# Kernel optimization log

Measured on AMD Instinct MI355X. Metric: run time of the kernel, lower is better.

Reference implementation:

```python
import jax, jax.numpy as jnp
import numpy as np

NEG_BIG = -1e9

def setup_inputs() -> dict:
    key = jax.random.key(0)
    kq, kk, kv, kwq, kwk, kwv, km = jax.random.split(key, 7)
    B, S, d = 16, 1024, 512
    Q = jax.random.normal(kq, (B, S, d), dtype=jnp.float32)
    K = jax.random.normal(kk, (B, S, d), dtype=jnp.float32)
    V = jax.random.normal(kv, (B, S, d), dtype=jnp.float32)
    # nn.Linear weights [d, d]; torch applies x @ W.T
    WQ = jax.random.normal(kwq, (d, d), dtype=jnp.float32) / np.sqrt(d)
    WK = jax.random.normal(kwk, (d, d), dtype=jnp.float32) / np.sqrt(d)
    WV = jax.random.normal(kwv, (d, d), dtype=jnp.float32) / np.sqrt(d)
    mask = jax.random.randint(km, (B, S), 0, 2, dtype=jnp.int32)
    return {"Q": Q, "K": K, "V": V, "WQ": WQ, "WK": WK, "WV": WV, "mask": mask}


def reference(Q, K, V, WQ, WK, WV, mask):
    d = Q.shape[-1]
    q = jnp.einsum('bsd,ed->bse', Q, WQ)
    k = jnp.einsum('bsd,ed->bse', K, WK)
    v = jnp.einsum('bsd,ed->bse', V, WV)
    scores = jnp.einsum('bqd,bkd->bqk', q, k) / jnp.sqrt(jnp.float32(d))
    attn = jax.nn.softmax(scores, axis=-1)
    # Faithful to original: mask applied AFTER softmax with -1e9 fill
    m = mask[:, None, :]  # [B,1,S] broadcast over query dim
    attn = jnp.where(m == 0, jnp.float32(NEG_BIG), attn)
    out = jnp.einsum('bqk,bkd->bqd', attn, v)
    return (out, attn)
```

## Files before the change

kernel.cpp:

```cpp
#include <hip/hip_runtime.h>
#include <hip/hip_bf16.h>

typedef float f32x4 __attribute__((ext_vector_type(4)));
typedef __bf16 bf16x8 __attribute__((ext_vector_type(8)));
typedef unsigned short u16x8 __attribute__((ext_vector_type(8)));
typedef unsigned short u16x4 __attribute__((ext_vector_type(4)));
typedef int i32x4 __attribute__((ext_vector_type(4)));

#define NEG_BIG_F (-1000000000.0f)
#define SCALE_F 0.044194173824159216f

__device__ __forceinline__ unsigned short f2bf(float f) {
  unsigned int u = __float_as_uint(f);
  u += 0x7FFFu + ((u >> 16) & 1u);
  return (unsigned short)(u >> 16);
}

__device__ __forceinline__ float bf2f(unsigned short h) {
  return __uint_as_float((unsigned int)h << 16);
}

__device__ __forceinline__ u16x8 cvt8(f32x4 a, f32x4 b) {
  u16x8 r;
  r[0] = f2bf(a[0]); r[1] = f2bf(a[1]); r[2] = f2bf(a[2]); r[3] = f2bf(a[3]);
  r[4] = f2bf(b[0]); r[5] = f2bf(b[1]); r[6] = f2bf(b[2]); r[7] = f2bf(b[3]);
  return r;
}

__device__ __forceinline__ bf16x8 u2b(u16x8 u) {
  union { u16x8 u; bf16x8 b; } c; c.u = u; return c.b;
}

__device__ __forceinline__ void gload16(const void* g, char* l) {
  __builtin_amdgcn_global_load_lds(
      (const __attribute__((address_space(1))) unsigned int*)g,
      (__attribute__((address_space(3))) unsigned int*)l, 16, 0, 0);
}

__global__ __launch_bounds__(256) void cvtWX(
    const float* __restrict__ w0, const float* __restrict__ w1,
    const float* __restrict__ w2, const float* __restrict__ Q,
    const float* __restrict__ Kx,
    unsigned short* __restrict__ wb, unsigned short* __restrict__ xb)
{
  const int z = blockIdx.z;
  if (z == 0) {
    if (blockIdx.x >= 384) return;
    const int i = (blockIdx.x * 256 + threadIdx.x) * 8;
    const float* src = i < 262144 ? w0 : (i < 524288 ? w1 : w2);
    const int j = i & 262143;
    f32x4 a = *(const f32x4*)(src + j);
    f32x4 b = *(const f32x4*)(src + j + 4);
    *(u16x8*)&wb[i] = cvt8(a, b);
  } else {
    const float* src = z == 1 ? Q : Kx;
    unsigned short* dst = xb + (size_t)(z - 1) * 8388608;
    const int i = (blockIdx.x * 256 + threadIdx.x) * 8;
    f32x4 a = *(const f32x4*)(src + i);
    f32x4 b = *(const f32x4*)(src + i + 4);
    *(u16x8*)&dst[i] = cvt8(a, b);
  }
}

__global__ __launch_bounds__(512, 2) void proj_all(
    const unsigned short* __restrict__ xb, const float* __restrict__ V,
    const unsigned short* __restrict__ wb,
    unsigned short* __restrict__ qb, unsigned short* __restrict__ kb,
    unsigned short* __restrict__ vt)
{
  __shared__ __align__(16) char pool[81920];

  const int bid = blockIdx.x;
  const int tid = threadIdx.x;
  const int lane = tid & 63, wave = tid >> 6;
  const int fr = lane & 15, fq = lane >> 4;

  if (bid < 256) {
    unsigned short (*As)[256][32] = (unsigned short (*)[256][32])pool;
    unsigned short (*Bs)[256][32] = (unsigned short (*)[256][32])(pool + 32768);

    const int z = bid >> 7, rem = bid & 127;
    const int m0 = (rem & 63) * 256, n0 = (rem >> 6) * 256;
    const unsigned short* Abase = xb + (size_t)z * 8388608 + (size_t)m0 * 512;
    const unsigned short* Bbase = wb + (size_t)z * 262144 + (size_t)n0 * 512;
    const int wr = (wave >> 2) * 128, wc = (wave & 3) * 64;

    f32x4 acc[8][4] = {};

    const unsigned short* gA[2]; char* lA[2];
    const unsigned short* gB[2]; char* lB[2];
    #pragma unroll
    for (int i = 0; i < 2; i++) {
      const int c = tid + 512 * i, row = c >> 2, slot = c & 3;
      const int sw = (slot ^ ((row >> 1) & 3)) * 8;
      gA[i] = Abase + (size_t)row * 512 + sw;
      gB[i] = Bbase + (size_t)row * 512 + sw;
      lA[i] = pool + c * 16;
      lB[i] = pool + 32768 + c * 16;
    }

    #pragma unroll
    for (int i = 0; i < 2; i++) { gload16(gA[i], lA[i]); gload16(gB[i], lB[i]); }

    int cur = 0;
    for (int kt = 0; kt < 512; kt += 32) {
      const int nb = cur ^ 1;
      if (kt < 480) {
        #pragma unroll
        for (int i = 0; i < 2; i++) {
          gload16(gA[i] + kt + 32, lA[i] + nb * 16384);
          gload16(gB[i] + kt + 32, lB[i] + nb * 16384);
        }
        asm volatile("s_waitcnt vmcnt(4) lgkmcnt(0)" ::: "memory");
      } else {
        asm volatile("s_waitcnt vmcnt(0) lgkmcnt(0)" ::: "memory");
      }
      __builtin_amdgcn_sched_barrier(0);
      __builtin_amdgcn_s_barrier();

      bf16x8 bv[4];
      #pragma unroll
      for (int nf = 0; nf < 4; nf++) {
        const int br = wc + nf * 16 + fr;
        bv[nf] = *(const bf16x8*)&Bs[cur][br][(fq ^ ((br >> 1) & 3)) * 8];
      }
      #pragma unroll
      for (int mf = 0; mf < 8; mf++) {
        const int ar = wr + mf * 16 + fr;
        bf16x8 av = *(const bf16x8*)&As[cur][ar][(fq ^ ((ar >> 1) & 3)) * 8];
        #pragma unroll
        for (int nf = 0; nf < 4; nf++)
          acc[mf][nf] = __builtin_amdgcn_mfma_f32_16x16x32_bf16(av, bv[nf], acc[mf][nf], 0, 0, 0);
      }
      __builtin_amdgcn_s_barrier();
      cur = nb;
    }

    unsigned short* Y = z ? kb : qb;
    #pragma unroll
    for (int mf = 0; mf < 8; mf++)
      #pragma unroll
      for (int nf = 0; nf < 4; nf++)
        #pragma unroll
        for (int rr = 0; rr < 4; rr++) {
          const int m = m0 + wr + mf * 16 + fq * 4 + rr;
          const int n = n0 + wc + nf * 16 + fr;
          Y[(size_t)m * 512 + n] = f2bf(acc[mf][nf][rr]);
        }
  } else {
    unsigned short (*As)[128][32] = (unsigned short (*)[128][32])pool;
    float          (*Bf)[256][32] = (float (*)[256][32])(pool + 16384);

    const int bid2 = bid - 256;
    const int m0 = (bid2 & 3) * 128, n0 = ((bid2 >> 2) & 3) * 256, b = bid2 >> 4;
    const int wr = (wave >> 2) * 64, wc = (wave & 3) * 64;
    const unsigned short* wv = wb + 524288;

    f32x4 acc[4][4] = {};

    const int arw = tid >> 2, asl = tid & 3;
    const unsigned short* gA = wv + (size_t)(m0 + arw) * 512 + (asl ^ ((arw >> 1) & 3)) * 8;
    char* lA = pool + tid * 16;
    const float* gB[4]; char* lB[4];
    #pragma unroll
    for (int i = 0; i < 4; i++) {
      const int c = tid + 512 * i, row = c >> 3, slot = c & 7;
      gB[i] = V + ((size_t)b * 1024 + n0 + row) * 512 + (slot ^ (row & 7)) * 4;
      lB[i] = pool + 16384 + c * 16;
    }

    gload16(gA, lA);
    #pragma unroll
    for (int i = 0; i < 4; i++) gload16(gB[i], lB[i]);

    int cur = 0;
    for (int kt = 0; kt < 512; kt += 32) {
      const int nb = cur ^ 1;
      if (kt < 480) {
        gload16(gA + kt + 32, lA + nb * 8192);
        #pragma unroll
        for (int i = 0; i < 4; i++) gload16(gB[i] + kt + 32, lB[i] + nb * 32768);
        asm volatile("s_waitcnt vmcnt(5) lgkmcnt(0)" ::: "memory");
      } else {
        asm volatile("s_waitcnt vmcnt(0) lgkmcnt(0)" ::: "memory");
      }
      __builtin_amdgcn_sched_barrier(0);
      __builtin_amdgcn_s_barrier();

      bf16x8 av[4], bv[4];
      #pragma unroll
      for (int mf = 0; mf < 4; mf++) {
        const int ar = wr + mf * 16 + fr;
        av[mf] = *(const bf16x8*)&As[cur][ar][(fq ^ ((ar >> 1) & 3)) * 8];
      }
      #pragma unroll
      for (int nf = 0; nf < 4; nf++) {
        const int br = wc + nf * 16 + fr;
        f32x4 lo = *(const f32x4*)&Bf[cur][br][((fq * 2)     ^ (br & 7)) * 4];
        f32x4 hi = *(const f32x4*)&Bf[cur][br][((fq * 2 + 1) ^ (br & 7)) * 4];
        bv[nf] = u2b(cvt8(lo, hi));
      }
      #pragma unroll
      for (int mf = 0; mf < 4; mf++)
        #pragma unroll
        for (int nf = 0; nf < 4; nf++)
          acc[mf][nf] = __builtin_amdgcn_mfma_f32_16x16x32_bf16(av[mf], bv[nf], acc[mf][nf], 0, 0, 0);
      __builtin_amdgcn_s_barrier();
      cur = nb;
    }

    #pragma unroll
    for (int mf = 0; mf < 4; mf++)
      #pragma unroll
      for (int nf = 0; nf < 4; nf++)
        #pragma unroll
        for (int rr = 0; rr < 4; rr++) {
          const int e = m0 + wr + mf * 16 + fq * 4 + rr;
          const int s = n0 + wc + nf * 16 + fr;
          vt[((size_t)b * 512 + e) * 1024 + s] = f2bf(acc[mf][nf][rr]);
        }
  }
}

__global__ __launch_bounds__(512, 2) void score_mv(
    const unsigned short* __restrict__ qb, const unsigned short* __restrict__ kb,
    const unsigned short* __restrict__ vt, const int* __restrict__ mask,
    unsigned short* __restrict__ P, float* __restrict__ partial,
    float* __restrict__ mvsum)
{
  __shared__ __align__(16) unsigned short As[2][256][32];
  __shared__ __align__(16) unsigned short Bs[2][256][32];

  const int bid = blockIdx.x;
  const int tid = threadIdx.x;

  if (bid >= 256) {
    const int row = (bid - 256) * 8 + (tid >> 6);
    const int b = row >> 9;
    const int lane = tid & 63;
    const unsigned short* vr = vt + (size_t)row * 1024 + lane * 16;
    const int* mr = mask + b * 1024 + lane * 16;
    u16x8 v0 = *(const u16x8*)(vr);
    u16x8 v1 = *(const u16x8*)(vr + 8);
    float s = 0.f;
    #pragma unroll
    for (int j = 0; j < 8; j++) {
      if (!mr[j])     s += bf2f(v0[j]);
      if (!mr[8 + j]) s += bf2f(v1[j]);
    }
    #pragma unroll
    for (int o = 32; o > 0; o >>= 1) s += __shfl_xor(s, o);
    if (lane == 0) mvsum[row] = s;
    return;
  }

  const int xcd = bid & 7, idx = bid >> 3;
  const int bz = xcd * 2 + (idx >> 4);
  const int tile = idx & 15;
  const int m0 = (tile & 3) * 256, n0 = ((tile >> 2) & 3) * 256;
  const int lane = tid & 63, wave = tid >> 6;
  const int wr = (wave >> 2) * 128, wc = (wave & 3) * 64;
  const int fr = lane & 15, fq = lane >> 4;

  f32x4 acc[8][4] = {};

  const unsigned short* gA[2]; char* lA[2];
  const unsigned short* gB[2]; char* lB[2];
  #pragma unroll
  for (int i = 0; i < 2; i++) {
    const int c = tid + 512 * i, row = c >> 2, slot = c & 3;
    const int sw = (slot ^ ((row >> 1) & 3)) * 8;
    gA[i] = qb + ((size_t)bz * 1024 + m0 + row) * 512 + sw;
    gB[i] = kb + ((size_t)bz * 1024 + n0 + row) * 512 + sw;
    lA[i] = (char*)&As[0][0][0] + c * 16;
    lB[i] = (char*)&Bs[0][0][0] + c * 16;
  }

  #pragma unroll
  for (int i = 0; i < 2; i++) { gload16(gA[i], lA[i]); gload16(gB[i], lB[i]); }

  int cur = 0;
  for (int kt = 0; kt < 512; kt += 32) {
    const int nb = cur ^ 1;
    if (kt < 480) {
      #pragma unroll
      for (int i = 0; i < 2; i++) {
        gload16(gA[i] + kt + 32, lA[i] + nb * 16384);
        gload16(gB[i] + kt + 32, lB[i] + nb * 16384);
      }
      asm volatile("s_waitcnt vmcnt(4) lgkmcnt(0)" ::: "memory");
    } else {
      asm volatile("s_waitcnt vmcnt(0) lgkmcnt(0)" ::: "memory");
    }
    __builtin_amdgcn_sched_barrier(0);
    __builtin_amdgcn_s_barrier();

    bf16x8 bv[4];
    #pragma unroll
    for (int nf = 0; nf < 4; nf++) {
      const int br = wc + nf * 16 + fr;
      bv[nf] = *(const bf16x8*)&Bs[cur][br][(fq ^ ((br >> 1) & 3)) * 8];
    }
    #pragma unroll
    for (int mf = 0; mf < 8; mf++) {
      const int ar = wr + mf * 16 + fr;
      bf16x8 av = *(const bf16x8*)&As[cur][ar][(fq ^ ((ar >> 1) & 3)) * 8];
      #pragma unroll
      for (int nf = 0; nf < 4; nf++)
        acc[mf][nf] = __builtin_amdgcn_mfma_f32_16x16x32_bf16(av, bv[nf], acc[mf][nf], 0, 0, 0);
    }
    __builtin_amdgcn_s_barrier();
    cur = nb;
  }

  int mcol[4];
  #pragma unroll
  for (int nf = 0; nf < 4; nf++)
    mcol[nf] = mask[bz * 1024 + n0 + wc + nf * 16 + fr];

  unsigned short* Pb = P + ((size_t)bz << 20);
  const int slot = ((tile >> 2) & 3) * 4 + (wave & 3);
  #pragma unroll
  for (int mf = 0; mf < 8; mf++) {
    #pragma unroll
    for (int rr = 0; rr < 4; rr++) {
      const int m = m0 + wr + mf * 16 + fq * 4 + rr;
      float e = 0.f;
      #pragma unroll
      for (int nf = 0; nf < 4; nf++) {
        const float ev = __expf(acc[mf][nf][rr] * SCALE_F);
        e += ev;
        Pb[(size_t)m * 1024 + n0 + wc + nf * 16 + fr] =
            mcol[nf] ? f2bf(ev) : (unsigned short)0;
      }
      e += __shfl_xor(e, 1); e += __shfl_xor(e, 2);
      e += __shfl_xor(e, 4); e += __shfl_xor(e, 8);
      if (fr == 0)
        partial[(size_t)slot * 16384 + bz * 1024 + m] = e;
    }
  }
}

__global__ __launch_bounds__(512) void pv_attn(
    const unsigned short* __restrict__ P, const unsigned short* __restrict__ vt,
    const float* __restrict__ partial, const float* __restrict__ mvsum,
    const int* __restrict__ mask,
    float* __restrict__ out, float* __restrict__ attn)
{
  __shared__ __align__(16) unsigned short As[2][64][32];
  __shared__ __align__(16) unsigned short Bs[2][512][32];
  __shared__ float inv_l[64];

  const int tid = threadIdx.x;
  const int lin = blockIdx.x;
  const int xcd = lin & 7, idx = lin >> 3;
  const int bz = xcd * 2 + (idx >> 4);
  const int m0 = (idx & 15) * 64;
  const int lane = tid & 63, wave = tid >> 6;
  const int n0 = wave * 64;
  const int fr = lane & 15, fq = lane >> 4;

  f32x4 acc[4][4] = {};

  if (tid < 64) {
    float s = 0.f;
    #pragma unroll
    for (int p = 0; p < 16; p++) s += partial[(size_t)p * 16384 + bz * 1024 + m0 + tid];
    inv_l[tid] = 1.0f / s;
  }

  const unsigned short* gA = nullptr; char* lA = nullptr;
  if (tid < 256) {
    const int row = tid >> 2, slot = tid & 3;
    gA = P + ((size_t)bz << 20) + (size_t)(m0 + row) * 1024 + (slot ^ ((row >> 1) & 3)) * 8;
    lA = (char*)&As[0][0][0] + tid * 16;
  }
  const unsigned short* gB[4]; char* lB[4];
  #pragma unroll
  for (int i = 0; i < 4; i++) {
    const int c = tid + 512 * i, row = c >> 2, slot = c & 3;
    gB[i] = vt + ((size_t)bz * 512 + row) * 1024 + (slot ^ ((row >> 1) & 3)) * 8;
    lB[i] = (char*)&Bs[0][0][0] + c * 16;
  }

  const int arow = tid >> 3, acol = (tid & 7) * 4;
  const int aslot8 = ((acol >> 3) ^ ((arow >> 1) & 3)) * 8 + (acol & 7);
  float* arp = attn + ((size_t)bz * 1024 + m0 + arow) * 1024 + acol;
  const int* mrp = mask + bz * 1024 + acol;

  if (tid < 256) gload16(gA, lA);
  #pragma unroll
  for (int i = 0; i < 4; i++) gload16(gB[i], lB[i]);
  __syncthreads();

  int cur = 0;
  for (int t = 0; t < 32; t++) {
    const int nb = cur ^ 1;
    const int kt = t * 32;
    if (t < 31) {
      if (tid < 256) gload16(gA + kt + 32, lA + nb * 4096);
      #pragma unroll
      for (int i = 0; i < 4; i++) gload16(gB[i] + kt + 32, lB[i] + nb * 32768);
      if (wave < 4) asm volatile("s_waitcnt vmcnt(5) lgkmcnt(0)" ::: "memory");
      else          asm volatile("s_waitcnt vmcnt(4) lgkmcnt(0)" ::: "memory");
    } else {
      asm volatile("s_waitcnt vmcnt(0) lgkmcnt(0)" ::: "memory");
    }
    __builtin_amdgcn_sched_barrier(0);
    __builtin_amdgcn_s_barrier();

    bf16x8 af[4], bv[4];
    #pragma unroll
    for (int mf = 0; mf < 4; mf++) {
      const int ar = mf * 16 + fr;
      af[mf] = *(const bf16x8*)&As[cur][ar][(fq ^ ((ar >> 1) & 3)) * 8];
    }
    #pragma unroll
    for (int nf = 0; nf < 4; nf++) {
      const int br = n0 + nf * 16 + fr;
      bv[nf] = *(const bf16x8*)&Bs[cur][br][(fq ^ ((br >> 1) & 3)) * 8];
    }
    #pragma unroll
    for (int mf = 0; mf < 4; mf++)
      #pragma unroll
      for (int nf = 0; nf < 4; nf++)
        acc[mf][nf] = __builtin_amdgcn_mfma_f32_16x16x32_bf16(af[mf], bv[nf], acc[mf][nf], 0, 0, 0);

    {
      const u16x4 pv4 = *(const u16x4*)&As[cur][arow][aslot8];
      const i32x4 mv = *(const i32x4*)(mrp + kt);
      const float iv = inv_l[arow];
      f32x4 o;
      o[0] = mv[0] ? bf2f(pv4[0]) * iv : NEG_BIG_F;
      o[1] = mv[1] ? bf2f(pv4[1]) * iv : NEG_BIG_F;
      o[2] = mv[2] ? bf2f(pv4[2]) * iv : NEG_BIG_F;
      o[3] = mv[3] ? bf2f(pv4[3]) * iv : NEG_BIG_F;
      *(f32x4*)(arp + kt) = o;
    }
    __builtin_amdgcn_s_barrier();
    cur = nb;
  }

  float mvv[4];
  #pragma unroll
  for (int nf = 0; nf < 4; nf++)
    mvv[nf] = mvsum[bz * 512 + n0 + nf * 16 + fr];
  #pragma unroll
  for (int mf = 0; mf < 4; mf++)
    #pragma unroll
    for (int rr = 0; rr < 4; rr++) {
      const int m = m0 + mf * 16 + fq * 4 + rr;
      const float iv = inv_l[mf * 16 + fq * 4 + rr];
      #pragma unroll
      for (int nf = 0; nf < 4; nf++)
        out[((size_t)bz * 1024 + m) * 512 + n0 + nf * 16 + fr] =
            iv * acc[mf][nf][rr] + NEG_BIG_F * mvv[nf];
    }
}

extern "C" void kernel_launch(void* const* d_in, const int* in_sizes, int n_in,
                              void* d_out, int out_size, void* d_ws, size_t ws_size,
                              hipStream_t stream)
{
  const float* Q  = (const float*)d_in[0];
  const float* Kx = (const float*)d_in[1];
  const float* V  = (const float*)d_in[2];
  const float* WQ = (const float*)d_in[3];
  const float* WK = (const float*)d_in[4];
  const float* WV = (const float*)d_in[5];
  const int* mask = (const int*)d_in[6];

  const int B = 16, S = 1024, D = 512;
  float* out_f  = (float*)d_out;
  float* attn_f = out_f + (size_t)B * S * D;
  unsigned short* Pbuf = (unsigned short*)d_out;
  unsigned short* xb = (unsigned short*)attn_f;

  unsigned short* qb = (unsigned short*)d_ws;
  unsigned short* kb = qb + (size_t)B * S * D;
  unsigned short* vt = kb + (size_t)B * S * D;
  unsigned short* wb = vt + (size_t)B * S * D;
  float* partial = (float*)(wb + 786432);
  float* mvsum = partial + 262144;

  cvtWX<<<dim3(4096, 1, 3), 256, 0, stream>>>(WQ, WK, WV, Q, Kx, wb, xb);
  proj_all<<<dim3(512), 512, 0, stream>>>(xb, V, wb, qb, kb, vt);
  score_mv<<<dim3(1280), 512, 0, stream>>>(qb, kb, vt, mask, Pbuf, partial, mvsum);
  pv_attn<<<dim3(256), 512, 0, stream>>>(Pbuf, vt, partial, mvsum, mask, out_f, attn_f);
}
```

Measured before the change: 137.2 us.

## Fuse Q/K fp32-to-bf16 conversion into projection GEMM loads

```diff
diff --git a/kernel.cpp b/kernel.cpp
--- a/kernel.cpp
+++ b/kernel.cpp
@@ -37,34 +37,21 @@
       (__attribute__((address_space(3))) unsigned int*)l, 16, 0, 0);
 }
 
-__global__ __launch_bounds__(256) void cvtWX(
+__global__ __launch_bounds__(256) void cvtW(
     const float* __restrict__ w0, const float* __restrict__ w1,
-    const float* __restrict__ w2, const float* __restrict__ Q,
-    const float* __restrict__ Kx,
-    unsigned short* __restrict__ wb, unsigned short* __restrict__ xb)
+    const float* __restrict__ w2, unsigned short* __restrict__ wb)
 {
-  const int z = blockIdx.z;
-  if (z == 0) {
-    if (blockIdx.x >= 384) return;
-    const int i = (blockIdx.x * 256 + threadIdx.x) * 8;
-    const float* src = i < 262144 ? w0 : (i < 524288 ? w1 : w2);
-    const int j = i & 262143;
-    f32x4 a = *(const f32x4*)(src + j);
-    f32x4 b = *(const f32x4*)(src + j + 4);
-    *(u16x8*)&wb[i] = cvt8(a, b);
-  } else {
-    const float* src = z == 1 ? Q : Kx;
-    unsigned short* dst = xb + (size_t)(z - 1) * 8388608;
-    const int i = (blockIdx.x * 256 + threadIdx.x) * 8;
-    f32x4 a = *(const f32x4*)(src + i);
-    f32x4 b = *(const f32x4*)(src + i + 4);
-    *(u16x8*)&dst[i] = cvt8(a, b);
-  }
+  const int i = (blockIdx.x * 256 + threadIdx.x) * 8;
+  const float* src = i < 262144 ? w0 : (i < 524288 ? w1 : w2);
+  const int j = i & 262143;
+  f32x4 a = *(const f32x4*)(src + j);
+  f32x4 b = *(const f32x4*)(src + j + 4);
+  *(u16x8*)&wb[i] = cvt8(a, b);
 }
 
 __global__ __launch_bounds__(512, 2) void proj_all(
-    const unsigned short* __restrict__ xb, const float* __restrict__ V,
-    const unsigned short* __restrict__ wb,
+    const float* __restrict__ Q, const float* __restrict__ Kx,
+    const float* __restrict__ V, const unsigned short* __restrict__ wb,
     unsigned short* __restrict__ qb, unsigned short* __restrict__ kb,
     unsigned short* __restrict__ vt)
 {
@@ -75,27 +62,31 @@
   const int lane = tid & 63, wave = tid >> 6;
   const int fr = lane & 15, fq = lane >> 4;
 
-  if (bid < 256) {
-    unsigned short (*As)[256][32] = (unsigned short (*)[256][32])pool;
+  if (bid < 512) {
+    float          (*Af)[128][32] = (float (*)[128][32])pool;
     unsigned short (*Bs)[256][32] = (unsigned short (*)[256][32])(pool + 32768);
 
-    const int z = bid >> 7, rem = bid & 127;
-    const int m0 = (rem & 63) * 256, n0 = (rem >> 6) * 256;
-    const unsigned short* Abase = xb + (size_t)z * 8388608 + (size_t)m0 * 512;
-    const unsigned short* Bbase = wb + (size_t)z * 262144 + (size_t)n0 * 512;
-    const int wr = (wave >> 2) * 128, wc = (wave & 3) * 64;
-
-    f32x4 acc[8][4] = {};
-
-    const unsigned short* gA[2]; char* lA[2];
+    const int z = bid >> 8, rem = bid & 255;
+    const float* X = z ? Kx : Q;
+    const unsigned short* W = wb + (size_t)z * 262144;
+    unsigned short* Y = z ? kb : qb;
+    const int m0 = (rem >> 1) * 128, n0 = (rem & 1) * 256;
+    const int wr = (wave >> 2) * 64, wc = (wave & 3) * 64;
+
+    f32x4 acc[4][4] = {};
+
+    const float* gA[2]; char* lA[2];
+    #pragma unroll
+    for (int i = 0; i < 2; i++) {
+      const int c = tid + 512 * i, row = c >> 3, slot = c & 7;
+      gA[i] = X + (size_t)(m0 + row) * 512 + (slot ^ (row & 7)) * 4;
+      lA[i] = pool + c * 16;
+    }
     const unsigned short* gB[2]; char* lB[2];
     #pragma unroll
     for (int i = 0; i < 2; i++) {
       const int c = tid + 512 * i, row = c >> 2, slot = c & 3;
-      const int sw = (slot ^ ((row >> 1) & 3)) * 8;
-      gA[i] = Abase + (size_t)row * 512 + sw;
-      gB[i] = Bbase + (size_t)row * 512 + sw;
-      lA[i] = pool + c * 16;
+      gB[i] = W + (size_t)(n0 + row) * 512 + (slot ^ ((row >> 1) & 3)) * 8;
       lB[i] = pool + 32768 + c * 16;
     }
 
@@ -118,27 +109,30 @@
       __builtin_amdgcn_sched_barrier(0);
       __builtin_amdgcn_s_barrier();
 
-      bf16x8 bv[4];
+      bf16x8 av[4], bv[4];
       #pragma unroll
       for (int nf = 0; nf < 4; nf++) {
         const int br = wc + nf * 16 + fr;
         bv[nf] = *(const bf16x8*)&Bs[cur][br][(fq ^ ((br >> 1) & 3)) * 8];
       }
       #pragma unroll
-      for (int mf = 0; mf < 8; mf++) {
+      for (int mf = 0; mf < 4; mf++) {
         const int ar = wr + mf * 16 + fr;
-        bf16x8 av = *(const bf16x8*)&As[cur][ar][(fq ^ ((ar >> 1) & 3)) * 8];
+        f32x4 lo = *(const f32x4*)&Af[cur][ar][((fq * 2)     ^ (ar & 7)) * 4];
+        f32x4 hi = *(const f32x4*)&Af[cur][ar][((fq * 2 + 1) ^ (ar & 7)) * 4];
+        av[mf] = u2b(cvt8(lo, hi));
+      }
+      #pragma unroll
+      for (int mf = 0; mf < 4; mf++)
         #pragma unroll
         for (int nf = 0; nf < 4; nf++)
-          acc[mf][nf] = __builtin_amdgcn_mfma_f32_16x16x32_bf16(av, bv[nf], acc[mf][nf], 0, 0, 0);
-      }
+          acc[mf][nf] = __builtin_amdgcn_mfma_f32_16x16x32_bf16(av[mf], bv[nf], acc[mf][nf], 0, 0, 0);
       __builtin_amdgcn_s_barrier();
       cur = nb;
     }
 
-    unsigned short* Y = z ? kb : qb;
-    #pragma unroll
-    for (int mf = 0; mf < 8; mf++)
+    #pragma unroll
+    for (int mf = 0; mf < 4; mf++)
       #pragma unroll
       for (int nf = 0; nf < 4; nf++)
         #pragma unroll
@@ -151,7 +145,7 @@
     unsigned short (*As)[128][32] = (unsigned short (*)[128][32])pool;
     float          (*Bf)[256][32] = (float (*)[256][32])(pool + 16384);
 
-    const int bid2 = bid - 256;
+    const int bid2 = bid - 512;
     const int m0 = (bid2 & 3) * 128, n0 = ((bid2 >> 2) & 3) * 256, b = bid2 >> 4;
     const int wr = (wave >> 2) * 64, wc = (wave & 3) * 64;
     const unsigned short* wv = wb + 524288;
@@ -474,7 +468,6 @@
   float* out_f  = (float*)d_out;
   float* attn_f = out_f + (size_t)B * S * D;
   unsigned short* Pbuf = (unsigned short*)d_out;
-  unsigned short* xb = (unsigned short*)attn_f;
 
   unsigned short* qb = (unsigned short*)d_ws;
   unsigned short* kb = qb + (size_t)B * S * D;
@@ -483,8 +476,8 @@
   float* partial = (float*)(wb + 786432);
   float* mvsum = partial + 262144;
 
-  cvtWX<<<dim3(4096, 1, 3), 256, 0, stream>>>(WQ, WK, WV, Q, Kx, wb, xb);
-  proj_all<<<dim3(512), 512, 0, stream>>>(xb, V, wb, qb, kb, vt);
+  cvtW<<<dim3(384), 256, 0, stream>>>(WQ, WK, WV, wb);
+  proj_all<<<dim3(768), 512, 0, stream>>>(Q, Kx, V, wb, qb, kb, vt);
   score_mv<<<dim3(1280), 512, 0, stream>>>(qb, kb, vt, mask, Pbuf, partial, mvsum);
   pv_attn<<<dim3(256), 512, 0, stream>>>(Pbuf, vt, partial, mvsum, mask, out_f, attn_f);
 }
```

After: 139.4 us. Within noise of the previous version (+1.6%).
